# Kernel optimization log

Hardware: AMD Instinct MI355X
Metric: run time of the kernel (lower is better)

Reference implementation:

```python
import jax, jax.numpy as jnp
import numpy as np

B, T, D, H, HD = 4, 2048, 1024, 16, 64
EPS = 1e-6


def _rotary_tables(seq_len, d_head):
    n = d_head // 4
    angular_freq = (1.0 / 1024) ** jnp.linspace(0, 1, n, dtype=jnp.float32)
    angular_freq = jnp.concatenate([angular_freq, jnp.zeros((n,), jnp.float32)])  # [d_head//2]
    theta = jnp.outer(jnp.arange(seq_len, dtype=jnp.float32), angular_freq)  # [T, d_head//2]
    return jnp.cos(theta), jnp.sin(theta)


def _apply_rotary(x, cos, sin):
    # x: [B, T, H, d]
    xf = x.astype(jnp.float32)
    x1, x2 = jnp.split(xf, 2, axis=-1)
    c = cos[None, :, None, :]
    s = sin[None, :, None, :]
    y1 = x1 * c + x2 * s
    y2 = -x1 * s + x2 * c
    return jnp.concatenate([y1, y2], axis=-1).astype(x.dtype)


def _rmsnorm(x, eps):
    return x * jax.lax.rsqrt(jnp.mean(x * x, axis=-1, keepdims=True) + eps)


def setup_inputs() -> dict:
    key = jax.random.key(0)
    ks = jax.random.split(key, 5)
    scale = 1.0 / np.sqrt(D)
    x = jax.random.normal(ks[0], (B, T, D), jnp.float32)
    wq = jax.random.normal(ks[1], (D, D), jnp.float32) * scale
    wk = jax.random.normal(ks[2], (D, D), jnp.float32) * scale
    wv = jax.random.normal(ks[3], (D, D), jnp.float32) * scale
    wo = jax.random.normal(ks[4], (D, D), jnp.float32) * scale
    mask = jnp.tril(jnp.ones((T, T), dtype=bool))  # causal
    return {"x": x, "wq": wq, "wk": wk, "wv": wv, "wo": wo, "mask": mask}


def reference(x, wq, wk, wv, wo, mask):
    # QKV projections (equinox Linear: y = x @ W.T)
    q = (x @ wq.T).reshape(B, T, H, HD)
    k = (x @ wk.T).reshape(B, T, H, HD)
    v = (x @ wv.T).reshape(B, T, H, HD)
    # QK-norm (RMS norm without weight)
    q = _rmsnorm(q, EPS)
    k = _rmsnorm(k, EPS)
    # Rotary embedding
    cos, sin = _rotary_tables(T, HD)
    q = _apply_rotary(q, cos, sin)
    k = _apply_rotary(k, cos, sin)
    # Attention
    scores = jnp.einsum('bshd,bthd->bhst', q, k) / jnp.sqrt(jnp.float32(HD))
    scores = jnp.where(mask[None, None, :, :], scores, -jnp.inf)
    weights = jax.nn.softmax(scores, axis=-1)
    out = jnp.einsum('bhst,bthd->bshd', weights, v)
    out = out.reshape(B, T, D)
    return out @ wo.T
```

## Files before the change

### kernel.cpp

```cpp
#include <hip/hip_runtime.h>
#include <hip/hip_bf16.h>
#include <math.h>

#define B_ 4
#define T_ 2048
#define D_ 1024
#define H_ 16
#define HD_ 64

typedef _Float16 f16x8 __attribute__((ext_vector_type(8)));
typedef _Float16 f16x4 __attribute__((ext_vector_type(4)));
typedef float f32x4 __attribute__((ext_vector_type(4)));

__device__ __forceinline__ void gload_lds16(const _Float16* g, _Float16* l) {
    __builtin_amdgcn_global_load_lds(
        (const __attribute__((address_space(1))) void*)g,
        (__attribute__((address_space(3))) void*)l,
        16, 0, 0);
}

__global__ __launch_bounds__(256) void castf(const float* __restrict__ in,
                                             _Float16* __restrict__ out, int n4) {
    const int i = blockIdx.x * 256 + threadIdx.x;
    if (i < n4) {
        const float4 v = ((const float4*)in)[i];
        f16x4 h = {(_Float16)v.x, (_Float16)v.y, (_Float16)v.z, (_Float16)v.w};
        ((f16x4*)out)[i] = h;
    }
}

__global__ __launch_bounds__(256) void castw(const float* __restrict__ a,
                                             const float* __restrict__ b,
                                             const float* __restrict__ c,
                                             const float* __restrict__ d,
                                             _Float16* __restrict__ oa,
                                             _Float16* __restrict__ ob,
                                             _Float16* __restrict__ oc,
                                             _Float16* __restrict__ od) {
    const int z = blockIdx.z;
    const float* in = (z == 0) ? a : (z == 1 ? b : (z == 2 ? c : d));
    _Float16* out = (z == 0) ? oa : (z == 1 ? ob : (z == 2 ? oc : od));
    const int i = blockIdx.x * 256 + threadIdx.x;
    const float4 v = ((const float4*)in)[i];
    f16x4 h = {(_Float16)v.x, (_Float16)v.y, (_Float16)v.z, (_Float16)v.w};
    ((f16x4*)out)[i] = h;
}

__global__ __launch_bounds__(256) void gemm_qkv(const _Float16* __restrict__ A,
                                                const _Float16* __restrict__ Wq,
                                                const _Float16* __restrict__ Wk,
                                                const _Float16* __restrict__ Wv,
                                                _Float16* __restrict__ qh,
                                                _Float16* __restrict__ kh,
                                                _Float16* __restrict__ vt) {
    constexpr int K = D_;
    const int z = blockIdx.z;
    const _Float16* W = (z == 0) ? Wq : (z == 1 ? Wk : Wv);
    __shared__ _Float16 As[128 * 32];
    __shared__ _Float16 Bs[128 * 32];
    const int tid = threadIdx.x;
    const int lane = tid & 63, w = tid >> 6;
    const int col = lane & 15, quad = lane >> 4;
    const int wm = w >> 1, wn = w & 1;
    const int row0 = blockIdx.y * 128, col0 = blockIdx.x * 128;
    const int sr = lane >> 2, sc = (lane & 3) * 8;

    f32x4 acc[4][4];
#pragma unroll
    for (int i = 0; i < 4; ++i)
#pragma unroll
        for (int j = 0; j < 4; ++j) acc[i][j] = (f32x4){0.f, 0.f, 0.f, 0.f};

    for (int kt = 0; kt < K / 32; ++kt) {
        const int k0 = kt * 32;
#pragma unroll
        for (int it = 0; it < 2; ++it) {
            const int rb = it * 64 + w * 16;
            gload_lds16(A + (size_t)(row0 + rb + sr) * K + k0 + sc, As + rb * 32);
            gload_lds16(W + (size_t)(col0 + rb + sr) * K + k0 + sc, Bs + rb * 32);
        }
        __syncthreads();
        f16x8 af[4], bf[4];
#pragma unroll
        for (int i = 0; i < 4; ++i) {
            af[i] = *(const f16x8*)&As[(wm * 64 + i * 16 + col) * 32 + quad * 8];
            bf[i] = *(const f16x8*)&Bs[(wn * 64 + i * 16 + col) * 32 + quad * 8];
        }
#pragma unroll
        for (int mi = 0; mi < 4; ++mi)
#pragma unroll
            for (int ni = 0; ni < 4; ++ni)
                acc[mi][ni] = __builtin_amdgcn_mfma_f32_16x16x32_f16(af[mi], bf[ni],
                                                                     acc[mi][ni], 0, 0, 0);
        __syncthreads();
    }

    if (z < 2) {
        _Float16* C = (z == 0) ? qh : kh;
        const float qscale = (z == 0) ? 0.18033688011112042f : 1.0f;
        const float fr = exp2f(-10.0f * (float)col * (1.0f / 15.0f));
#pragma unroll
        for (int mi = 0; mi < 4; ++mi) {
            float ssq[4];
#pragma unroll
            for (int r = 0; r < 4; ++r) {
                float t = 0.f;
#pragma unroll
                for (int ni = 0; ni < 4; ++ni) t += acc[mi][ni][r] * acc[mi][ni][r];
                ssq[r] = t;
            }
#pragma unroll
            for (int st = 1; st < 16; st <<= 1)
#pragma unroll
                for (int r = 0; r < 4; ++r) ssq[r] += __shfl_xor(ssq[r], st, 64);
            const int rowb = row0 + wm * 64 + mi * 16 + quad * 4;
#pragma unroll
            for (int r = 0; r < 4; ++r) {
                const float scl = rsqrtf(ssq[r] * (1.0f / 64.0f) + 1e-6f) * qscale;
                const int t = (rowb + r) & (T_ - 1);
                float s, c;
                sincosf((float)t * fr, &s, &c);
                const float x0 = acc[mi][0][r] * scl;
                const float x1 = acc[mi][1][r] * scl;
                const float x2 = acc[mi][2][r] * scl;
                const float x3 = acc[mi][3][r] * scl;
                const float y0 = fmaf(x0, c, x2 * s);
                const float y2 = fmaf(x2, c, -x0 * s);
                const size_t base = (size_t)(rowb + r) * D_ + col0 + wn * 64 + col;
                C[base + 0]  = (_Float16)y0;
                C[base + 16] = (_Float16)x1;
                C[base + 32] = (_Float16)y2;
                C[base + 48] = (_Float16)x3;
            }
        }
    } else {
        const int hh = blockIdx.x * 2 + wn;
#pragma unroll
        for (int mi = 0; mi < 4; ++mi) {
            const int row = row0 + wm * 64 + mi * 16 + quad * 4;
            const int bb = row >> 11;
            const int t0m = row & (T_ - 1);
#pragma unroll
            for (int ni = 0; ni < 4; ++ni) {
                const int d = ni * 16 + col;
                f16x4 pk = {(_Float16)acc[mi][ni][0], (_Float16)acc[mi][ni][1],
                            (_Float16)acc[mi][ni][2], (_Float16)acc[mi][ni][3]};
                *(f16x4*)&vt[((size_t)(bb * H_ + hh) * HD_ + d) * T_ + t0m] = pk;
            }
        }
    }
}

__global__ __launch_bounds__(256) void gemm_wo(const _Float16* __restrict__ A,
                                               const _Float16* __restrict__ W,
                                               float* __restrict__ C) {
    constexpr int K = D_, N = D_;
    __shared__ _Float16 As[128 * 32];
    __shared__ _Float16 Bs[128 * 32];
    const int tid = threadIdx.x;
    const int lane = tid & 63, w = tid >> 6;
    const int col = lane & 15, quad = lane >> 4;
    const int wm = w >> 1, wn = w & 1;
    const int row0 = blockIdx.y * 128, col0 = blockIdx.x * 128;
    const int sr = lane >> 2, sc = (lane & 3) * 8;

    f32x4 acc[4][4];
#pragma unroll
    for (int i = 0; i < 4; ++i)
#pragma unroll
        for (int j = 0; j < 4; ++j) acc[i][j] = (f32x4){0.f, 0.f, 0.f, 0.f};

    for (int kt = 0; kt < K / 32; ++kt) {
        const int k0 = kt * 32;
#pragma unroll
        for (int it = 0; it < 2; ++it) {
            const int rb = it * 64 + w * 16;
            gload_lds16(A + (size_t)(row0 + rb + sr) * K + k0 + sc, As + rb * 32);
            gload_lds16(W + (size_t)(col0 + rb + sr) * K + k0 + sc, Bs + rb * 32);
        }
        __syncthreads();
        f16x8 af[4], bf[4];
#pragma unroll
        for (int i = 0; i < 4; ++i) {
            af[i] = *(const f16x8*)&As[(wm * 64 + i * 16 + col) * 32 + quad * 8];
            bf[i] = *(const f16x8*)&Bs[(wn * 64 + i * 16 + col) * 32 + quad * 8];
        }
#pragma unroll
        for (int mi = 0; mi < 4; ++mi)
#pragma unroll
            for (int ni = 0; ni < 4; ++ni)
                acc[mi][ni] = __builtin_amdgcn_mfma_f32_16x16x32_f16(af[mi], bf[ni],
                                                                     acc[mi][ni], 0, 0, 0);
        __syncthreads();
    }
#pragma unroll
    for (int mi = 0; mi < 4; ++mi)
#pragma unroll
        for (int ni = 0; ni < 4; ++ni)
#pragma unroll
            for (int r = 0; r < 4; ++r)
                C[(size_t)(row0 + wm * 64 + mi * 16 + quad * 4 + r) * N +
                  col0 + wn * 64 + ni * 16 + col] = acc[mi][ni][r];
}

#define LDP 88

__global__ __launch_bounds__(512) void flash_mfma(const _Float16* __restrict__ qh,
                                                  const _Float16* __restrict__ kh,
                                                  const _Float16* __restrict__ vt,
                                                  _Float16* __restrict__ o) {
    __shared__ _Float16 Kl[2][64 * 64];
    __shared__ _Float16 Vl[2][64 * 64];
    __shared__ _Float16 Pl[8][16 * LDP];
    const int tid = threadIdx.x;
    const int lane = tid & 63, w = tid >> 6;
    const int col = lane & 15, quad = lane >> 4;
    const int bh = blockIdx.x, b = bh >> 4, h = bh & 15;
    const int srow = lane >> 3;
    const int schunk = (lane & 7) ^ srow;
    const int sw = col & 7;
    const int rstg = w * 8 + srow;

    const _Float16* kbase = kh + ((size_t)b * T_ * H_ + (size_t)h) * HD_;
    const _Float16* vbase = vt + ((size_t)(b * H_ + h)) * (size_t)HD_ * T_;

    for (int phase = 0; phase < 2; ++phase) {
        const int qt = (phase == 0) ? (int)blockIdx.y : (15 - (int)blockIdx.y);
        const int q0 = qt * 128;

        const int tq = q0 + w * 16 + col;
        const _Float16* qp = qh + ((size_t)(b * T_ + tq) * H_ + h) * HD_ + quad * 8;
        const f16x8 qB0 = *(const f16x8*)(qp);
        const f16x8 qB1 = *(const f16x8*)(qp + 32);

        f32x4 oa[4];
#pragma unroll
        for (int i = 0; i < 4; ++i) oa[i] = (f32x4){0.f, 0.f, 0.f, 0.f};
        float l_ = 0.f;

        const int nkt = 2 * qt + 2;

        gload_lds16(kbase + (size_t)(0 + rstg) * H_ * HD_ + schunk * 8,
                    &Kl[0][(w * 8) * 64]);
        gload_lds16(vbase + (size_t)rstg * T_ + 0 + schunk * 8,
                    &Vl[0][(w * 8) * 64]);
        __builtin_amdgcn_sched_barrier(0);
        asm volatile("s_waitcnt vmcnt(0)" ::: "memory");
        __builtin_amdgcn_sched_barrier(0);
        __builtin_amdgcn_s_barrier();

        for (int kt = 0; kt < nkt; ++kt) {
            const int k0 = kt * 64;
            const int cur = kt & 1;

            if (kt + 1 < nkt) {
                gload_lds16(kbase + (size_t)(k0 + 64 + rstg) * H_ * HD_ + schunk * 8,
                            &Kl[cur ^ 1][(w * 8) * 64]);
                gload_lds16(vbase + (size_t)rstg * T_ + k0 + 64 + schunk * 8,
                            &Vl[cur ^ 1][(w * 8) * 64]);
            }

            f32x4 s[4];
            __builtin_amdgcn_s_setprio(1);
#pragma unroll
            for (int tn = 0; tn < 4; ++tn) {
                const _Float16* kp = &Kl[cur][(tn * 16 + col) * 64];
                const f16x8 kA0 = *(const f16x8*)(kp + ((quad ^ sw) << 3));
                const f16x8 kA1 = *(const f16x8*)(kp + (((quad | 4) ^ sw) << 3));
                f32x4 a = (f32x4){0.f, 0.f, 0.f, 0.f};
                a = __builtin_amdgcn_mfma_f32_16x16x32_f16(kA0, qB0, a, 0, 0, 0);
                a = __builtin_amdgcn_mfma_f32_16x16x32_f16(kA1, qB1, a, 0, 0, 0);
                s[tn] = a;
            }
            __builtin_amdgcn_s_setprio(0);

            if (k0 + 63 > q0 + w * 16) {
                const int qq = q0 + w * 16 + col;
#pragma unroll
                for (int tn = 0; tn < 4; ++tn)
#pragma unroll
                    for (int r = 0; r < 4; ++r) {
                        const int key = k0 + tn * 16 + quad * 4 + r;
                        if (key > qq) s[tn][r] = -1e30f;
                    }
            }

#pragma unroll
            for (int tn = 0; tn < 4; ++tn) {
                f16x4 pk;
#pragma unroll
                for (int r = 0; r < 4; ++r) {
                    const float p = exp2f(s[tn][r]);
                    l_ += p;
                    pk[r] = (_Float16)p;
                }
                *(f16x4*)&Pl[w][col * LDP + tn * 16 + quad * 4] = pk;
            }

            const f16x8 pA0 = *(const f16x8*)&Pl[w][col * LDP + quad * 8];
            const f16x8 pA1 = *(const f16x8*)&Pl[w][col * LDP + quad * 8 + 32];
            __builtin_amdgcn_s_setprio(1);
#pragma unroll
            for (int tn = 0; tn < 4; ++tn) {
                const _Float16* vp = &Vl[cur][(tn * 16 + col) * 64];
                const f16x8 vB0 = *(const f16x8*)(vp + ((quad ^ sw) << 3));
                const f16x8 vB1 = *(const f16x8*)(vp + (((quad | 4) ^ sw) << 3));
                oa[tn] = __builtin_amdgcn_mfma_f32_16x16x32_f16(pA0, vB0, oa[tn], 0, 0, 0);
                oa[tn] = __builtin_amdgcn_mfma_f32_16x16x32_f16(pA1, vB1, oa[tn], 0, 0, 0);
            }
            __builtin_amdgcn_s_setprio(0);

            __builtin_amdgcn_sched_barrier(0);
            asm volatile("s_waitcnt vmcnt(0)" ::: "memory");
            __builtin_amdgcn_sched_barrier(0);
            __builtin_amdgcn_s_barrier();
        }

        l_ += __shfl_xor(l_, 16, 64);
        l_ += __shfl_xor(l_, 32, 64);
        const float linv = 1.0f / l_;
        float inv[4];
#pragma unroll
        for (int r = 0; r < 4; ++r) inv[r] = __shfl(linv, quad * 4 + r, 64);
#pragma unroll
        for (int tn = 0; tn < 4; ++tn)
#pragma unroll
            for (int r = 0; r < 4; ++r)
                o[((size_t)(b * T_ + q0 + w * 16 + quad * 4 + r) * H_ + h) * HD_ + tn * 16 + col] =
                    (_Float16)(oa[tn][r] * inv[r]);
    }
}

extern "C" void kernel_launch(void* const* d_in, const int* in_sizes, int n_in,
                              void* d_out, int out_size, void* d_ws, size_t ws_size,
                              hipStream_t stream) {
    const float* x  = (const float*)d_in[0];
    const float* wq = (const float*)d_in[1];
    const float* wk = (const float*)d_in[2];
    const float* wv = (const float*)d_in[3];
    const float* wo = (const float*)d_in[4];
    float* out = (float*)d_out;

    const size_t NE = (size_t)B_ * T_ * D_;
    const size_t WE = (size_t)D_ * D_;
    _Float16* xh  = (_Float16*)d_ws;
    _Float16* qh  = xh + NE;
    _Float16* kh  = qh + NE;
    _Float16* vth = kh + NE;
    _Float16* oh  = vth + NE;
    _Float16* wqh = oh + NE;
    _Float16* wkh = wqh + WE;
    _Float16* wvh = wkh + WE;
    _Float16* woh = wvh + WE;

    castf<<<NE / 1024, 256, 0, stream>>>(x, xh, (int)(NE / 4));
    castw<<<dim3(WE / 1024, 1, 4), 256, 0, stream>>>(wq, wk, wv, wo,
                                                     wqh, wkh, wvh, woh);

    gemm_qkv<<<dim3(D_ / 128, (B_ * T_) / 128, 3), 256, 0, stream>>>(
        xh, wqh, wkh, wvh, qh, kh, vth);

    flash_mfma<<<dim3(B_ * H_, 8, 1), 512, 0, stream>>>(qh, kh, vth, oh);

    gemm_wo<<<dim3(D_ / 128, (B_ * T_) / 128, 1), 256, 0, stream>>>(oh, woh, out);
}
```

Baseline: 275.3 us.

## Give each flash-attention wave two query sub-tiles with four waves per block

The flash kernel drops from 8 waves of 16 query rows to 4 waves of 32 query rows each. Each wave now reuses every K and V fragment it reads from LDS for two MFMA streams, and each thread stages twice as many K/V rows. This halves LDS K/V read traffic per query, at the cost of more registers per wave and fewer waves available to hide latency.

```diff
diff --git a/kernel.cpp b/kernel.cpp
--- a/kernel.cpp
+++ b/kernel.cpp
@@ -205,13 +205,13 @@
 
 #define LDP 88
 
-__global__ __launch_bounds__(512) void flash_mfma(const _Float16* __restrict__ qh,
+__global__ __launch_bounds__(256) void flash_mfma(const _Float16* __restrict__ qh,
                                                   const _Float16* __restrict__ kh,
                                                   const _Float16* __restrict__ vt,
                                                   _Float16* __restrict__ o) {
     __shared__ _Float16 Kl[2][64 * 64];
     __shared__ _Float16 Vl[2][64 * 64];
-    __shared__ _Float16 Pl[8][16 * LDP];
+    __shared__ _Float16 Pl[4][2][16 * LDP];
     const int tid = threadIdx.x;
     const int lane = tid & 63, w = tid >> 6;
     const int col = lane & 15, quad = lane >> 4;
@@ -219,31 +219,43 @@
     const int srow = lane >> 3;
     const int schunk = (lane & 7) ^ srow;
     const int sw = col & 7;
-    const int rstg = w * 8 + srow;
+    const int r1 = w * 8 + srow;
+    const int r2 = 32 + w * 8 + srow;
 
     const _Float16* kbase = kh + ((size_t)b * T_ * H_ + (size_t)h) * HD_;
     const _Float16* vbase = vt + ((size_t)(b * H_ + h)) * (size_t)HD_ * T_;
+
+#define STAGE_KV(buf, kk)                                                           \
+    gload_lds16(kbase + (size_t)((kk) + r1) * (H_ * HD_) + schunk * 8,              \
+                &Kl[buf][(w * 8) * 64]);                                            \
+    gload_lds16(kbase + (size_t)((kk) + r2) * (H_ * HD_) + schunk * 8,              \
+                &Kl[buf][(32 + w * 8) * 64]);                                       \
+    gload_lds16(vbase + (size_t)r1 * T_ + (kk) + schunk * 8,                        \
+                &Vl[buf][(w * 8) * 64]);                                            \
+    gload_lds16(vbase + (size_t)r2 * T_ + (kk) + schunk * 8,                        \
+                &Vl[buf][(32 + w * 8) * 64])
 
     for (int phase = 0; phase < 2; ++phase) {
         const int qt = (phase == 0) ? (int)blockIdx.y : (15 - (int)blockIdx.y);
         const int q0 = qt * 128;
-
-        const int tq = q0 + w * 16 + col;
-        const _Float16* qp = qh + ((size_t)(b * T_ + tq) * H_ + h) * HD_ + quad * 8;
-        const f16x8 qB0 = *(const f16x8*)(qp);
-        const f16x8 qB1 = *(const f16x8*)(qp + 32);
-
-        f32x4 oa[4];
-#pragma unroll
-        for (int i = 0; i < 4; ++i) oa[i] = (f32x4){0.f, 0.f, 0.f, 0.f};
-        float l_ = 0.f;
+        const int qw = q0 + w * 32;
+
+        const _Float16* qpA = qh + ((size_t)(b * T_ + qw + col) * H_ + h) * HD_ + quad * 8;
+        const _Float16* qpB = qh + ((size_t)(b * T_ + qw + 16 + col) * H_ + h) * HD_ + quad * 8;
+        const f16x8 qA0 = *(const f16x8*)(qpA), qA1 = *(const f16x8*)(qpA + 32);
+        const f16x8 qB0 = *(const f16x8*)(qpB), qB1 = *(const f16x8*)(qpB + 32);
+
+        f32x4 oa0[4], oa1[4];
+#pragma unroll
+        for (int i = 0; i < 4; ++i) {
+            oa0[i] = (f32x4){0.f, 0.f, 0.f, 0.f};
+            oa1[i] = (f32x4){0.f, 0.f, 0.f, 0.f};
+        }
+        float l0 = 0.f, l1 = 0.f;
 
         const int nkt = 2 * qt + 2;
 
-        gload_lds16(kbase + (size_t)(0 + rstg) * H_ * HD_ + schunk * 8,
-                    &Kl[0][(w * 8) * 64]);
-        gload_lds16(vbase + (size_t)rstg * T_ + 0 + schunk * 8,
-                    &Vl[0][(w * 8) * 64]);
+        STAGE_KV(0, 0);
         __builtin_amdgcn_sched_barrier(0);
         asm volatile("s_waitcnt vmcnt(0)" ::: "memory");
         __builtin_amdgcn_sched_barrier(0);
@@ -254,13 +266,10 @@
             const int cur = kt & 1;
 
             if (kt + 1 < nkt) {
-                gload_lds16(kbase + (size_t)(k0 + 64 + rstg) * H_ * HD_ + schunk * 8,
-                            &Kl[cur ^ 1][(w * 8) * 64]);
-                gload_lds16(vbase + (size_t)rstg * T_ + k0 + 64 + schunk * 8,
-                            &Vl[cur ^ 1][(w * 8) * 64]);
-            }
-
-            f32x4 s[4];
+                STAGE_KV(cur ^ 1, k0 + 64);
+            }
+
+            f32x4 s0[4], s1[4];
             __builtin_amdgcn_s_setprio(1);
 #pragma unroll
             for (int tn = 0; tn < 4; ++tn) {
@@ -268,45 +277,67 @@
                 const f16x8 kA0 = *(const f16x8*)(kp + ((quad ^ sw) << 3));
                 const f16x8 kA1 = *(const f16x8*)(kp + (((quad | 4) ^ sw) << 3));
                 f32x4 a = (f32x4){0.f, 0.f, 0.f, 0.f};
-                a = __builtin_amdgcn_mfma_f32_16x16x32_f16(kA0, qB0, a, 0, 0, 0);
-                a = __builtin_amdgcn_mfma_f32_16x16x32_f16(kA1, qB1, a, 0, 0, 0);
-                s[tn] = a;
+                a = __builtin_amdgcn_mfma_f32_16x16x32_f16(kA0, qA0, a, 0, 0, 0);
+                a = __builtin_amdgcn_mfma_f32_16x16x32_f16(kA1, qA1, a, 0, 0, 0);
+                s0[tn] = a;
+                f32x4 bb = (f32x4){0.f, 0.f, 0.f, 0.f};
+                bb = __builtin_amdgcn_mfma_f32_16x16x32_f16(kA0, qB0, bb, 0, 0, 0);
+                bb = __builtin_amdgcn_mfma_f32_16x16x32_f16(kA1, qB1, bb, 0, 0, 0);
+                s1[tn] = bb;
             }
             __builtin_amdgcn_s_setprio(0);
 
-            if (k0 + 63 > q0 + w * 16) {
-                const int qq = q0 + w * 16 + col;
+            if (k0 + 63 > qw) {
+                const int qq = qw + col;
 #pragma unroll
                 for (int tn = 0; tn < 4; ++tn)
 #pragma unroll
                     for (int r = 0; r < 4; ++r) {
                         const int key = k0 + tn * 16 + quad * 4 + r;
-                        if (key > qq) s[tn][r] = -1e30f;
+                        if (key > qq) s0[tn][r] = -1e30f;
                     }
             }
+            if (k0 + 63 > qw + 16) {
+                const int qq = qw + 16 + col;
+#pragma unroll
+                for (int tn = 0; tn < 4; ++tn)
+#pragma unroll
+                    for (int r = 0; r < 4; ++r) {
+                        const int key = k0 + tn * 16 + quad * 4 + r;
+                        if (key > qq) s1[tn][r] = -1e30f;
+                    }
+            }
 
 #pragma unroll
             for (int tn = 0; tn < 4; ++tn) {
-                f16x4 pk;
+                f16x4 pk0, pk1;
 #pragma unroll
                 for (int r = 0; r < 4; ++r) {
-                    const float p = exp2f(s[tn][r]);
-                    l_ += p;
-                    pk[r] = (_Float16)p;
+                    const float p0 = exp2f(s0[tn][r]);
+                    l0 += p0;
+                    pk0[r] = (_Float16)p0;
+                    const float p1 = exp2f(s1[tn][r]);
+                    l1 += p1;
+                    pk1[r] = (_Float16)p1;
                 }
-                *(f16x4*)&Pl[w][col * LDP + tn * 16 + quad * 4] = pk;
-            }
-
-            const f16x8 pA0 = *(const f16x8*)&Pl[w][col * LDP + quad * 8];
-            const f16x8 pA1 = *(const f16x8*)&Pl[w][col * LDP + quad * 8 + 32];
+                *(f16x4*)&Pl[w][0][col * LDP + tn * 16 + quad * 4] = pk0;
+                *(f16x4*)&Pl[w][1][col * LDP + tn * 16 + quad * 4] = pk1;
+            }
+
+            const f16x8 pA0a = *(const f16x8*)&Pl[w][0][col * LDP + quad * 8];
+            const f16x8 pA1a = *(const f16x8*)&Pl[w][0][col * LDP + quad * 8 + 32];
+            const f16x8 pA0b = *(const f16x8*)&Pl[w][1][col * LDP + quad * 8];
+            const f16x8 pA1b = *(const f16x8*)&Pl[w][1][col * LDP + quad * 8 + 32];
             __builtin_amdgcn_s_setprio(1);
 #pragma unroll
             for (int tn = 0; tn < 4; ++tn) {
                 const _Float16* vp = &Vl[cur][(tn * 16 + col) * 64];
                 const f16x8 vB0 = *(const f16x8*)(vp + ((quad ^ sw) << 3));
                 const f16x8 vB1 = *(const f16x8*)(vp + (((quad | 4) ^ sw) << 3));
-                oa[tn] = __builtin_amdgcn_mfma_f32_16x16x32_f16(pA0, vB0, oa[tn], 0, 0, 0);
-                oa[tn] = __builtin_amdgcn_mfma_f32_16x16x32_f16(pA1, vB1, oa[tn], 0, 0, 0);
+                oa0[tn] = __builtin_amdgcn_mfma_f32_16x16x32_f16(pA0a, vB0, oa0[tn], 0, 0, 0);
+                oa0[tn] = __builtin_amdgcn_mfma_f32_16x16x32_f16(pA1a, vB1, oa0[tn], 0, 0, 0);
+                oa1[tn] = __builtin_amdgcn_mfma_f32_16x16x32_f16(pA0b, vB0, oa1[tn], 0, 0, 0);
+                oa1[tn] = __builtin_amdgcn_mfma_f32_16x16x32_f16(pA1b, vB1, oa1[tn], 0, 0, 0);
             }
             __builtin_amdgcn_s_setprio(0);
 
@@ -316,19 +347,29 @@
             __builtin_amdgcn_s_barrier();
         }
 
-        l_ += __shfl_xor(l_, 16, 64);
-        l_ += __shfl_xor(l_, 32, 64);
-        const float linv = 1.0f / l_;
-        float inv[4];
-#pragma unroll
-        for (int r = 0; r < 4; ++r) inv[r] = __shfl(linv, quad * 4 + r, 64);
+        l0 += __shfl_xor(l0, 16, 64);
+        l0 += __shfl_xor(l0, 32, 64);
+        l1 += __shfl_xor(l1, 16, 64);
+        l1 += __shfl_xor(l1, 32, 64);
+        const float linv0 = 1.0f / l0;
+        const float linv1 = 1.0f / l1;
+        float inv0[4], inv1[4];
+#pragma unroll
+        for (int r = 0; r < 4; ++r) {
+            inv0[r] = __shfl(linv0, quad * 4 + r, 64);
+            inv1[r] = __shfl(linv1, quad * 4 + r, 64);
+        }
 #pragma unroll
         for (int tn = 0; tn < 4; ++tn)
 #pragma unroll
-            for (int r = 0; r < 4; ++r)
-                o[((size_t)(b * T_ + q0 + w * 16 + quad * 4 + r) * H_ + h) * HD_ + tn * 16 + col] =
-                    (_Float16)(oa[tn][r] * inv[r]);
+            for (int r = 0; r < 4; ++r) {
+                o[((size_t)(b * T_ + qw + quad * 4 + r) * H_ + h) * HD_ + tn * 16 + col] =
+                    (_Float16)(oa0[tn][r] * inv0[r]);
+                o[((size_t)(b * T_ + qw + 16 + quad * 4 + r) * H_ + h) * HD_ + tn * 16 + col] =
+                    (_Float16)(oa1[tn][r] * inv1[r]);
+            }
     }
+#undef STAGE_KV
 }
 
 extern "C" void kernel_launch(void* const* d_in, const int* in_sizes, int n_in,
@@ -360,7 +401,7 @@
     gemm_qkv<<<dim3(D_ / 128, (B_ * T_) / 128, 3), 256, 0, stream>>>(
         xh, wqh, wkh, wvh, qh, kh, vth);
 
-    flash_mfma<<<dim3(B_ * H_, 8, 1), 512, 0, stream>>>(qh, kh, vth, oh);
+    flash_mfma<<<dim3(B_ * H_, 8, 1), 256, 0, stream>>>(qh, kh, vth, oh);
 
     gemm_wo<<<dim3(D_ / 128, (B_ * T_) / 128, 1), 256, 0, stream>>>(oh, woh, out);
 }
```

Measured after the change: 293.1 us. 1.06x slower.
